# Optimization experiments

Hardware: AMD Instinct MI355X
Metric: run time of the kernel (lower is better)

The kernel has to match this reference:

```python
import jax, jax.numpy as jnp
import numpy as np

NUM_ITERS = 3


def squash(s, axis=-1):
    # v = (|s|^2 / (1+|s|^2)) * s / |s|
    sq = jnp.sum(s * s, axis=axis, keepdims=True)
    return sq / (1.0 + sq) * s / jnp.sqrt(sq)


def setup_inputs() -> dict:
    key = jax.random.key(0)
    k1, k2 = jax.random.split(key)
    B, C, R, I, O = 256, 10, 1152, 8, 16
    x = jax.random.normal(k1, (B, R, I), dtype=jnp.float32)
    route_weights = jax.random.normal(k2, (C, R, I, O), dtype=jnp.float32)
    return {"x": x, "route_weights": route_weights}


def reference(x, route_weights):
    # x: [B, R, I]; route_weights: [C, R, I, O]
    # u: predictions from each route node for each output capsule: [B, C, R, 1, O]
    u = jnp.einsum("bri,crio->bcro", x, route_weights)[:, :, :, None, :]
    b = jnp.zeros_like(u)
    v = None
    for i in range(NUM_ITERS):
        c = jax.nn.softmax(b, axis=2)          # softmax over route nodes (dim=2)
        s = jnp.sum(c * u, axis=2, keepdims=True)  # [B, C, 1, 1, O]
        v = squash(s, axis=-1)
        if i != NUM_ITERS - 1:
            b = b + jnp.sum(u * v, axis=-1, keepdims=True)  # agreement, broadcast over O
    return v  # [B, C, 1, 1, O]
```

## Files before the change

### kernel.cpp

```cpp
#include <hip/hip_runtime.h>
#include <stdint.h>


#define B_ 256
#define C_ 10
#define R_ 1152
#define I_ 8
#define O_ 16
#define T_ 512
#define KPT 9
#define NW 8
#define NITER 3

typedef float f32x4 __attribute__((ext_vector_type(4)));

__device__ __forceinline__ uint32_t bf16_rn(float f) {
    uint32_t u = __builtin_bit_cast(uint32_t, f);
    return (u + 0x7FFFu + ((u >> 16) & 1u)) >> 16;
}
__device__ __forceinline__ uint32_t pack2(float lo, float hi) {
    return bf16_rn(lo) | (bf16_rn(hi) << 16);
}
__device__ __forceinline__ float unlo(uint32_t p) {
    return __builtin_bit_cast(float, p << 16);
}
__device__ __forceinline__ float unhi(uint32_t p) {
    return __builtin_bit_cast(float, p & 0xFFFF0000u);
}

__global__ __launch_bounds__(T_, 3) void caps_u_kernel(
    const float* __restrict__ x,
    const float* __restrict__ w,
    uint2* __restrict__ u)
{
    const int bx  = blockIdx.x;
    const int c   = bx / 288;
    const int kc  = (bx % 288) >> 5;
    const int bt  = bx & 31;
    const int tid = threadIdx.x;
    const int oq  = tid & 3;
    const int rl  = tid >> 2;
    const int r   = kc * 128 + rl;

    const float* wbase = w + ((size_t)c * R_ + r) * (I_ * O_) + oq * 4;
    f32x4 W0, W1, W2, W3, W4, W5, W6, W7;
    asm volatile("global_load_dwordx4 %0, %1, off"            : "=v"(W0) : "v"(wbase));
    asm volatile("global_load_dwordx4 %0, %1, off offset:64"  : "=v"(W1) : "v"(wbase));
    asm volatile("global_load_dwordx4 %0, %1, off offset:128" : "=v"(W2) : "v"(wbase));
    asm volatile("global_load_dwordx4 %0, %1, off offset:192" : "=v"(W3) : "v"(wbase));
    asm volatile("global_load_dwordx4 %0, %1, off offset:256" : "=v"(W4) : "v"(wbase));
    asm volatile("global_load_dwordx4 %0, %1, off offset:320" : "=v"(W5) : "v"(wbase));
    asm volatile("global_load_dwordx4 %0, %1, off offset:384" : "=v"(W6) : "v"(wbase));
    asm volatile("global_load_dwordx4 %0, %1, off offset:448" : "=v"(W7) : "v"(wbase));
    asm volatile("s_waitcnt vmcnt(0)"
                 : "+v"(W0), "+v"(W1), "+v"(W2), "+v"(W3),
                   "+v"(W4), "+v"(W5), "+v"(W6), "+v"(W7));

    #pragma unroll 4
    for (int bb = 0; bb < 8; ++bb) {
        const int b = bt * 8 + bb;
        const float4* xp = (const float4*)(x + ((size_t)b * R_ + r) * I_);
        const float4 xa = xp[0];
        const float4 xb = xp[1];
        float a0, a1, a2, a3;
        a0 = xa.x * W0[0]; a1 = xa.x * W0[1]; a2 = xa.x * W0[2]; a3 = xa.x * W0[3];
        a0 += xa.y * W1[0]; a1 += xa.y * W1[1]; a2 += xa.y * W1[2]; a3 += xa.y * W1[3];
        a0 += xa.z * W2[0]; a1 += xa.z * W2[1]; a2 += xa.z * W2[2]; a3 += xa.z * W2[3];
        a0 += xa.w * W3[0]; a1 += xa.w * W3[1]; a2 += xa.w * W3[2]; a3 += xa.w * W3[3];
        a0 += xb.x * W4[0]; a1 += xb.x * W4[1]; a2 += xb.x * W4[2]; a3 += xb.x * W4[3];
        a0 += xb.y * W5[0]; a1 += xb.y * W5[1]; a2 += xb.y * W5[2]; a3 += xb.y * W5[3];
        a0 += xb.z * W6[0]; a1 += xb.z * W6[1]; a2 += xb.z * W6[2]; a3 += xb.z * W6[3];
        a0 += xb.w * W7[0]; a1 += xb.w * W7[1]; a2 += xb.w * W7[2]; a3 += xb.w * W7[3];
        u[(((size_t)b * C_ + c) * KPT + kc) * T_ + tid] =
            make_uint2(pack2(a0, a1), pack2(a2, a3));
    }
}

__global__ __launch_bounds__(T_, 4) void caps_route_kernel(
    const uint2* __restrict__ u,
    float* __restrict__ out)
{
    const int wg   = blockIdx.x;
    const int tid  = threadIdx.x;
    const int lane = tid & 63;
    const int wid  = tid >> 6;
    const int oq   = tid & 3;

    __shared__ float sred[NW][4][4];
    __shared__ float zred[NW];
    __shared__ float vsum[O_];

    uint2 up[KPT];
    #pragma unroll
    for (int k = 0; k < KPT; ++k)
        up[k] = u[((size_t)wg * KPT + k) * T_ + tid];

    if (tid < O_) vsum[tid] = 0.f;
    __syncthreads();

    #pragma unroll
    for (int it = 0; it < NITER; ++it) {
        float4 vs = make_float4(0.f, 0.f, 0.f, 0.f);
        if (it > 0) vs = *(const float4*)&vsum[oq * 4];
        float z = 0.f, s0 = 0.f, s1 = 0.f, s2 = 0.f, s3 = 0.f;
        #pragma unroll
        for (int k = 0; k < KPT; ++k) {
            const float u0 = unlo(up[k].x);
            const float u1 = unhi(up[k].x);
            const float u2 = unlo(up[k].y);
            const float u3 = unhi(up[k].y);
            float e;
            if (it == 0) {
                e = 1.f;
            } else {
                float d = u0 * vs.x + u1 * vs.y + u2 * vs.z + u3 * vs.w;
                d += __shfl_xor(d, 1);
                d += __shfl_xor(d, 2);
                e = __expf(d);
            }
            z += e;
            s0 += e * u0; s1 += e * u1; s2 += e * u2; s3 += e * u3;
        }
        #pragma unroll
        for (int off = 4; off <= 32; off <<= 1) {
            z  += __shfl_xor(z, off);
            s0 += __shfl_xor(s0, off);
            s1 += __shfl_xor(s1, off);
            s2 += __shfl_xor(s2, off);
            s3 += __shfl_xor(s3, off);
        }
        if (lane < 4) {
            sred[wid][lane][0] = s0;
            sred[wid][lane][1] = s1;
            sred[wid][lane][2] = s2;
            sred[wid][lane][3] = s3;
            if (lane == 0) zred[wid] = z;
        }
        __syncthreads();

        if (wid == 0 && lane < O_) {
            float S = 0.f, Z = 0.f;
            #pragma unroll
            for (int wv = 0; wv < NW; ++wv) {
                S += sred[wv][lane >> 2][lane & 3];
                Z += zred[wv];
            }
            const float inv = 1.f / Z;
            const float svn = S * inv;
            float p = svn * svn;
            p += __shfl_xor(p, 1);
            p += __shfl_xor(p, 2);
            p += __shfl_xor(p, 4);
            p += __shfl_xor(p, 8);
            const float scale = sqrtf(p) / (1.f + p);
            const float vf = svn * scale;
            vsum[lane] += vf;
            if (it == NITER - 1)
                out[(size_t)wg * O_ + lane] = vf;
        }
        if (it != NITER - 1) __syncthreads();
    }
}

#define BPB 4
#define RPP 128

__global__ __launch_bounds__(T_, 2) void capsule_fused_kernel(
    const float* __restrict__ x,
    const float* __restrict__ w,
    float* __restrict__ out)
{
    const int wg   = blockIdx.x;
    const int c    = wg >> 6;
    const int b0   = (wg & 63) * BPB;
    const int tid  = threadIdx.x;
    const int lane = tid & 63;
    const int wid  = tid >> 6;
    const int oq   = tid & 3;
    const int rl   = tid >> 2;

    __shared__ float sred[BPB][NW][4][4];
    __shared__ float zred[BPB][NW];
    __shared__ float vsum[BPB][O_];

    uint32_t up[BPB][KPT][2];

    if (tid < BPB * O_) vsum[tid >> 4][tid & 15] = 0.f;

    #pragma unroll
    for (int k = 0; k < KPT; ++k) {
        const int r = k * RPP + rl;
        const float4* wb4 = (const float4*)(w + ((size_t)c * R_ + r) * (I_ * O_));
        float4 W0 = wb4[0 * 4 + oq], W1 = wb4[1 * 4 + oq];
        float4 W2 = wb4[2 * 4 + oq], W3 = wb4[3 * 4 + oq];
        float4 W4 = wb4[4 * 4 + oq], W5 = wb4[5 * 4 + oq];
        float4 W6 = wb4[6 * 4 + oq], W7 = wb4[7 * 4 + oq];
        #pragma unroll
        for (int bb = 0; bb < BPB; ++bb) {
            const float4* xp = (const float4*)(x + ((size_t)(b0 + bb) * R_ + r) * I_);
            const float4 xa = xp[0];
            const float4 xb = xp[1];
            float a0, a1, a2, a3;
            a0 = xa.x * W0.x; a1 = xa.x * W0.y; a2 = xa.x * W0.z; a3 = xa.x * W0.w;
            a0 += xa.y * W1.x; a1 += xa.y * W1.y; a2 += xa.y * W1.z; a3 += xa.y * W1.w;
            a0 += xa.z * W2.x; a1 += xa.z * W2.y; a2 += xa.z * W2.z; a3 += xa.z * W2.w;
            a0 += xa.w * W3.x; a1 += xa.w * W3.y; a2 += xa.w * W3.z; a3 += xa.w * W3.w;
            a0 += xb.x * W4.x; a1 += xb.x * W4.y; a2 += xb.x * W4.z; a3 += xb.x * W4.w;
            a0 += xb.y * W5.x; a1 += xb.y * W5.y; a2 += xb.y * W5.z; a3 += xb.y * W5.w;
            a0 += xb.z * W6.x; a1 += xb.z * W6.y; a2 += xb.z * W6.z; a3 += xb.z * W6.w;
            a0 += xb.w * W7.x; a1 += xb.w * W7.y; a2 += xb.w * W7.z; a3 += xb.w * W7.w;
            up[bb][k][0] = pack2(a0, a1);
            up[bb][k][1] = pack2(a2, a3);
        }
    }
    __syncthreads();

    #pragma unroll
    for (int it = 0; it < NITER; ++it) {
        float zz[BPB], ss[BPB][4];
        #pragma unroll
        for (int bb = 0; bb < BPB; ++bb) {
            float4 vs = make_float4(0.f, 0.f, 0.f, 0.f);
            if (it > 0) vs = *(const float4*)&vsum[bb][oq * 4];
            float z = 0.f, s0 = 0.f, s1 = 0.f, s2 = 0.f, s3 = 0.f;
            #pragma unroll
            for (int k = 0; k < KPT; ++k) {
                const float u0 = unlo(up[bb][k][0]);
                const float u1 = unhi(up[bb][k][0]);
                const float u2 = unlo(up[bb][k][1]);
                const float u3 = unhi(up[bb][k][1]);
                float e;
                if (it == 0) {
                    e = 1.f;
                } else {
                    float d = u0 * vs.x + u1 * vs.y + u2 * vs.z + u3 * vs.w;
                    d += __shfl_xor(d, 1);
                    d += __shfl_xor(d, 2);
                    e = __expf(d);
                }
                z += e;
                s0 += e * u0; s1 += e * u1; s2 += e * u2; s3 += e * u3;
            }
            zz[bb] = z;
            ss[bb][0] = s0; ss[bb][1] = s1; ss[bb][2] = s2; ss[bb][3] = s3;
        }
        #pragma unroll
        for (int off = 4; off <= 32; off <<= 1) {
            #pragma unroll
            for (int bb = 0; bb < BPB; ++bb) {
                zz[bb] += __shfl_xor(zz[bb], off);
                ss[bb][0] += __shfl_xor(ss[bb][0], off);
                ss[bb][1] += __shfl_xor(ss[bb][1], off);
                ss[bb][2] += __shfl_xor(ss[bb][2], off);
                ss[bb][3] += __shfl_xor(ss[bb][3], off);
            }
        }
        if (lane < 4) {
            #pragma unroll
            for (int bb = 0; bb < BPB; ++bb) {
                sred[bb][wid][lane][0] = ss[bb][0];
                sred[bb][wid][lane][1] = ss[bb][1];
                sred[bb][wid][lane][2] = ss[bb][2];
                sred[bb][wid][lane][3] = ss[bb][3];
                if (lane == 0) zred[bb][wid] = zz[bb];
            }
        }
        __syncthreads();

        if (wid == 0) {
            const int bb = lane >> 4;
            const int o  = lane & 15;
            float S = 0.f, Z = 0.f;
            #pragma unroll
            for (int wv = 0; wv < NW; ++wv) {
                S += sred[bb][wv][o >> 2][o & 3];
                Z += zred[bb][wv];
            }
            const float inv = 1.f / Z;
            const float svn = S * inv;
            float p = svn * svn;
            p += __shfl_xor(p, 1);
            p += __shfl_xor(p, 2);
            p += __shfl_xor(p, 4);
            p += __shfl_xor(p, 8);
            const float scale = sqrtf(p) / (1.f + p);
            const float vf = svn * scale;
            vsum[bb][o] += vf;
            if (it == NITER - 1)
                out[((size_t)(b0 + bb) * C_ + c) * O_ + o] = vf;
        }
        if (it != NITER - 1) __syncthreads();
    }
}

extern "C" void kernel_launch(void* const* d_in, const int* in_sizes, int n_in,
                              void* d_out, int out_size, void* d_ws, size_t ws_size,
                              hipStream_t stream) {
    const float* x = (const float*)d_in[0];
    const float* w = (const float*)d_in[1];
    float* out = (float*)d_out;

    const size_t u_bytes = (size_t)B_ * C_ * KPT * T_ * 8;
    if (ws_size >= u_bytes) {
        uint2* u = (uint2*)d_ws;
        caps_u_kernel<<<dim3(C_ * KPT * 32), dim3(T_), 0, stream>>>(x, w, u);
        caps_route_kernel<<<dim3(B_ * C_), dim3(T_), 0, stream>>>(u, out);
    } else {
        capsule_fused_kernel<<<dim3(C_ * (B_ / BPB)), dim3(T_), 0, stream>>>(x, w, out);
    }
}
```

Before: 61.83 us.

## Stage x in LDS, pack two batches per u record, route two batches per block

The u-producing kernel now stages its 8-batch x tile into 32 KB of shared memory with coalesced float4 loads instead of each thread reading x directly. It also interleaves u for batch pairs into 16-byte records. The routing kernel then processes two batches per workgroup with wider uint4 loads, halving the grid and amortising the barriers and reductions over two batches. The costs are extra LDS use that may limit occupancy, higher register pressure in routing, and an occupancy hint lowered from 4 to 3.

```diff
diff --git a/kernel.cpp b/kernel.cpp
--- a/kernel.cpp
+++ b/kernel.cpp
@@ -31,16 +31,31 @@
 __global__ __launch_bounds__(T_, 3) void caps_u_kernel(
     const float* __restrict__ x,
     const float* __restrict__ w,
-    uint2* __restrict__ u)
+    uint4* __restrict__ u)
 {
     const int bx  = blockIdx.x;
     const int c   = bx / 288;
     const int kc  = (bx % 288) >> 5;
     const int bt  = bx & 31;
+    const int b0  = bt * 8;
     const int tid = threadIdx.x;
     const int oq  = tid & 3;
     const int rl  = tid >> 2;
     const int r   = kc * 128 + rl;
+
+    __shared__ float xs[8 * 1024];
+
+    {
+        const float* xg = x + (size_t)b0 * (R_ * I_) + kc * 1024;
+        #pragma unroll
+        for (int j = 0; j < 8; ++j) {
+            const int e  = j * 512 + tid;
+            const int bb = e >> 8;
+            const int q  = e & 255;
+            const float4 v = *(const float4*)(xg + (size_t)bb * (R_ * I_) + q * 4);
+            *(float4*)&xs[e * 4] = v;
+        }
+    }
 
     const float* wbase = w + ((size_t)c * R_ + r) * (I_ * O_) + oq * 4;
     f32x4 W0, W1, W2, W3, W4, W5, W6, W7;
@@ -56,94 +71,112 @@
                  : "+v"(W0), "+v"(W1), "+v"(W2), "+v"(W3),
                    "+v"(W4), "+v"(W5), "+v"(W6), "+v"(W7));
 
-    #pragma unroll 4
-    for (int bb = 0; bb < 8; ++bb) {
-        const int b = bt * 8 + bb;
-        const float4* xp = (const float4*)(x + ((size_t)b * R_ + r) * I_);
-        const float4 xa = xp[0];
-        const float4 xb = xp[1];
-        float a0, a1, a2, a3;
-        a0 = xa.x * W0[0]; a1 = xa.x * W0[1]; a2 = xa.x * W0[2]; a3 = xa.x * W0[3];
-        a0 += xa.y * W1[0]; a1 += xa.y * W1[1]; a2 += xa.y * W1[2]; a3 += xa.y * W1[3];
-        a0 += xa.z * W2[0]; a1 += xa.z * W2[1]; a2 += xa.z * W2[2]; a3 += xa.z * W2[3];
-        a0 += xa.w * W3[0]; a1 += xa.w * W3[1]; a2 += xa.w * W3[2]; a3 += xa.w * W3[3];
-        a0 += xb.x * W4[0]; a1 += xb.x * W4[1]; a2 += xb.x * W4[2]; a3 += xb.x * W4[3];
-        a0 += xb.y * W5[0]; a1 += xb.y * W5[1]; a2 += xb.y * W5[2]; a3 += xb.y * W5[3];
-        a0 += xb.z * W6[0]; a1 += xb.z * W6[1]; a2 += xb.z * W6[2]; a3 += xb.z * W6[3];
-        a0 += xb.w * W7[0]; a1 += xb.w * W7[1]; a2 += xb.w * W7[2]; a3 += xb.w * W7[3];
-        u[(((size_t)b * C_ + c) * KPT + kc) * T_ + tid] =
-            make_uint2(pack2(a0, a1), pack2(a2, a3));
-    }
-}
-
-__global__ __launch_bounds__(T_, 4) void caps_route_kernel(
-    const uint2* __restrict__ u,
+    __syncthreads();
+
+    const size_t ubase = (((size_t)(bt * 4) * C_ + c) * KPT + kc) * T_ + tid;
+
+    #pragma unroll
+    for (int p = 0; p < 4; ++p) {
+        uint32_t lo0, lo1, hi0, hi1;
+        #pragma unroll
+        for (int h = 0; h < 2; ++h) {
+            const int bb = p * 2 + h;
+            const float4 xa = *(const float4*)&xs[(bb * 128 + rl) * 8];
+            const float4 xb = *(const float4*)&xs[(bb * 128 + rl) * 8 + 4];
+            float a0, a1, a2, a3;
+            a0 = xa.x * W0[0]; a1 = xa.x * W0[1]; a2 = xa.x * W0[2]; a3 = xa.x * W0[3];
+            a0 += xa.y * W1[0]; a1 += xa.y * W1[1]; a2 += xa.y * W1[2]; a3 += xa.y * W1[3];
+            a0 += xa.z * W2[0]; a1 += xa.z * W2[1]; a2 += xa.z * W2[2]; a3 += xa.z * W2[3];
+            a0 += xa.w * W3[0]; a1 += xa.w * W3[1]; a2 += xa.w * W3[2]; a3 += xa.w * W3[3];
+            a0 += xb.x * W4[0]; a1 += xb.x * W4[1]; a2 += xb.x * W4[2]; a3 += xb.x * W4[3];
+            a0 += xb.y * W5[0]; a1 += xb.y * W5[1]; a2 += xb.y * W5[2]; a3 += xb.y * W5[3];
+            a0 += xb.z * W6[0]; a1 += xb.z * W6[1]; a2 += xb.z * W6[2]; a3 += xb.z * W6[3];
+            a0 += xb.w * W7[0]; a1 += xb.w * W7[1]; a2 += xb.w * W7[2]; a3 += xb.w * W7[3];
+            if (h == 0) { lo0 = pack2(a0, a1); lo1 = pack2(a2, a3); }
+            else        { hi0 = pack2(a0, a1); hi1 = pack2(a2, a3); }
+        }
+        u[ubase + (size_t)p * (C_ * KPT * T_)] = make_uint4(lo0, lo1, hi0, hi1);
+    }
+}
+
+__global__ __launch_bounds__(T_, 3) void caps_route_kernel(
+    const uint4* __restrict__ u,
     float* __restrict__ out)
 {
-    const int wg   = blockIdx.x;
+    const int wg2  = blockIdx.x;
+    const int b2   = wg2 / C_;
+    const int c    = wg2 % C_;
     const int tid  = threadIdx.x;
     const int lane = tid & 63;
     const int wid  = tid >> 6;
     const int oq   = tid & 3;
 
-    __shared__ float sred[NW][4][4];
-    __shared__ float zred[NW];
-    __shared__ float vsum[O_];
-
-    uint2 up[KPT];
+    __shared__ float sred[2][NW][4][4];
+    __shared__ float zred[2][NW];
+    __shared__ float vsum[2][O_];
+
+    uint4 up[KPT];
     #pragma unroll
     for (int k = 0; k < KPT; ++k)
-        up[k] = u[((size_t)wg * KPT + k) * T_ + tid];
-
-    if (tid < O_) vsum[tid] = 0.f;
+        up[k] = u[((size_t)wg2 * KPT + k) * T_ + tid];
+
+    if (tid < 2 * O_) vsum[tid >> 4][tid & 15] = 0.f;
     __syncthreads();
 
     #pragma unroll
     for (int it = 0; it < NITER; ++it) {
-        float4 vs = make_float4(0.f, 0.f, 0.f, 0.f);
-        if (it > 0) vs = *(const float4*)&vsum[oq * 4];
-        float z = 0.f, s0 = 0.f, s1 = 0.f, s2 = 0.f, s3 = 0.f;
+        float4 vs0 = make_float4(0.f, 0.f, 0.f, 0.f);
+        float4 vs1 = vs0;
+        if (it > 0) {
+            vs0 = *(const float4*)&vsum[0][oq * 4];
+            vs1 = *(const float4*)&vsum[1][oq * 4];
+        }
+        float z0 = 0.f, s00 = 0.f, s01 = 0.f, s02 = 0.f, s03 = 0.f;
+        float z1 = 0.f, s10 = 0.f, s11 = 0.f, s12 = 0.f, s13 = 0.f;
         #pragma unroll
         for (int k = 0; k < KPT; ++k) {
-            const float u0 = unlo(up[k].x);
-            const float u1 = unhi(up[k].x);
-            const float u2 = unlo(up[k].y);
-            const float u3 = unhi(up[k].y);
-            float e;
+            const float u00 = unlo(up[k].x), u01 = unhi(up[k].x);
+            const float u02 = unlo(up[k].y), u03 = unhi(up[k].y);
+            const float u10 = unlo(up[k].z), u11 = unhi(up[k].z);
+            const float u12 = unlo(up[k].w), u13 = unhi(up[k].w);
+            float e0, e1;
             if (it == 0) {
-                e = 1.f;
+                e0 = 1.f; e1 = 1.f;
             } else {
-                float d = u0 * vs.x + u1 * vs.y + u2 * vs.z + u3 * vs.w;
-                d += __shfl_xor(d, 1);
-                d += __shfl_xor(d, 2);
-                e = __expf(d);
-            }
-            z += e;
-            s0 += e * u0; s1 += e * u1; s2 += e * u2; s3 += e * u3;
+                float d0 = u00 * vs0.x + u01 * vs0.y + u02 * vs0.z + u03 * vs0.w;
+                float d1 = u10 * vs1.x + u11 * vs1.y + u12 * vs1.z + u13 * vs1.w;
+                d0 += __shfl_xor(d0, 1); d1 += __shfl_xor(d1, 1);
+                d0 += __shfl_xor(d0, 2); d1 += __shfl_xor(d1, 2);
+                e0 = __expf(d0); e1 = __expf(d1);
+            }
+            z0 += e0; s00 += e0 * u00; s01 += e0 * u01; s02 += e0 * u02; s03 += e0 * u03;
+            z1 += e1; s10 += e1 * u10; s11 += e1 * u11; s12 += e1 * u12; s13 += e1 * u13;
         }
         #pragma unroll
         for (int off = 4; off <= 32; off <<= 1) {
-            z  += __shfl_xor(z, off);
-            s0 += __shfl_xor(s0, off);
-            s1 += __shfl_xor(s1, off);
-            s2 += __shfl_xor(s2, off);
-            s3 += __shfl_xor(s3, off);
+            z0 += __shfl_xor(z0, off);   z1 += __shfl_xor(z1, off);
+            s00 += __shfl_xor(s00, off); s01 += __shfl_xor(s01, off);
+            s02 += __shfl_xor(s02, off); s03 += __shfl_xor(s03, off);
+            s10 += __shfl_xor(s10, off); s11 += __shfl_xor(s11, off);
+            s12 += __shfl_xor(s12, off); s13 += __shfl_xor(s13, off);
         }
         if (lane < 4) {
-            sred[wid][lane][0] = s0;
-            sred[wid][lane][1] = s1;
-            sred[wid][lane][2] = s2;
-            sred[wid][lane][3] = s3;
-            if (lane == 0) zred[wid] = z;
+            sred[0][wid][lane][0] = s00; sred[0][wid][lane][1] = s01;
+            sred[0][wid][lane][2] = s02; sred[0][wid][lane][3] = s03;
+            sred[1][wid][lane][0] = s10; sred[1][wid][lane][1] = s11;
+            sred[1][wid][lane][2] = s12; sred[1][wid][lane][3] = s13;
+            if (lane == 0) { zred[0][wid] = z0; zred[1][wid] = z1; }
         }
         __syncthreads();
 
-        if (wid == 0 && lane < O_) {
+        if (wid == 0 && lane < 2 * O_) {
+            const int bb = lane >> 4;
+            const int o  = lane & 15;
             float S = 0.f, Z = 0.f;
             #pragma unroll
             for (int wv = 0; wv < NW; ++wv) {
-                S += sred[wv][lane >> 2][lane & 3];
-                Z += zred[wv];
+                S += sred[bb][wv][o >> 2][o & 3];
+                Z += zred[bb][wv];
             }
             const float inv = 1.f / Z;
             const float svn = S * inv;
@@ -154,9 +187,9 @@
             p += __shfl_xor(p, 8);
             const float scale = sqrtf(p) / (1.f + p);
             const float vf = svn * scale;
-            vsum[lane] += vf;
+            vsum[bb][o] += vf;
             if (it == NITER - 1)
-                out[(size_t)wg * O_ + lane] = vf;
+                out[((size_t)(b2 * 2 + bb) * C_ + c) * O_ + o] = vf;
         }
         if (it != NITER - 1) __syncthreads();
     }
@@ -300,11 +333,11 @@
     const float* w = (const float*)d_in[1];
     float* out = (float*)d_out;
 
-    const size_t u_bytes = (size_t)B_ * C_ * KPT * T_ * 8;
+    const size_t u_bytes = (size_t)(B_ / 2) * C_ * KPT * T_ * 16;
     if (ws_size >= u_bytes) {
-        uint2* u = (uint2*)d_ws;
+        uint4* u = (uint4*)d_ws;
         caps_u_kernel<<<dim3(C_ * KPT * 32), dim3(T_), 0, stream>>>(x, w, u);
-        caps_route_kernel<<<dim3(B_ * C_), dim3(T_), 0, stream>>>(u, out);
+        caps_route_kernel<<<dim3((B_ / 2) * C_), dim3(T_), 0, stream>>>(u, out);
     } else {
         capsule_fused_kernel<<<dim3(C_ * (B_ / BPB)), dim3(T_), 0, stream>>>(x, w, out);
     }
```

Result: slower. 67.11 us (+8.5%).
